# Performance work log

Hardware: AMD Instinct MI355X
Metric: run time of the kernel (lower is better)

Reference implementation:

```python
import jax, jax.numpy as jnp
import numpy as np

B, L, D_IN, H, N2, NL, D_OUT = 32, 4096, 16, 128, 32, 4, 8


def setup_inputs() -> dict:
    key = jax.random.key(0)
    ks = jax.random.split(key, 12)
    x = jax.random.normal(ks[0], (B, L, D_IN), jnp.float32)
    times = jax.random.uniform(ks[1], (B, L), jnp.float32)
    enc_w = jax.random.normal(ks[2], (H, D_IN), jnp.float32) / np.sqrt(D_IN)
    enc_b = jnp.zeros((H,), jnp.float32)
    # S4D kernel params per layer (stacked along NL)
    log_dt = jax.random.uniform(ks[3], (NL, H), jnp.float32) * (np.log(0.1) - np.log(0.001)) + np.log(0.001)
    log_A_real = jnp.full((NL, H, N2), np.log(0.5), jnp.float32)
    A_imag = jnp.broadcast_to(np.pi * jnp.arange(N2, dtype=jnp.float32), (NL, H, N2)).astype(jnp.float32)
    C_re = jax.random.normal(ks[4], (NL, H, N2), jnp.float32) * (0.5 ** 0.5)
    C_im = jax.random.normal(ks[5], (NL, H, N2), jnp.float32) * (0.5 ** 0.5)
    D = jax.random.normal(ks[6], (NL, H), jnp.float32)
    conv_w = jax.random.normal(ks[7], (NL, 2 * H, H), jnp.float32) / np.sqrt(H)  # 1x1 conv
    conv_b = jnp.zeros((NL, 2 * H), jnp.float32)
    ln_w = jnp.ones((NL, H), jnp.float32)
    ln_b = jnp.zeros((NL, H), jnp.float32)
    dec_w = jax.random.normal(ks[8], (D_OUT, H), jnp.float32) / np.sqrt(H)
    dec_b = jnp.zeros((D_OUT,), jnp.float32)
    return dict(x=x, times=times, enc_w=enc_w, enc_b=enc_b, log_dt=log_dt,
                log_A_real=log_A_real, A_imag=A_imag, C_re=C_re, C_im=C_im, D=D,
                conv_w=conv_w, conv_b=conv_b, ln_w=ln_w, ln_b=ln_b, dec_w=dec_w, dec_b=dec_b)


def _s4d_kernel(log_dt, log_A_real, A_imag, C_re, C_im, L_):
    # Vandermonde construction of the S4D convolution kernel, shape (H, L)
    dt = jnp.exp(log_dt)[:, None]                      # (H, 1)
    A = -jnp.exp(log_A_real) + 1j * A_imag             # (H, N2)
    dtA = A * dt                                       # (H, N2)
    C = (C_re + 1j * C_im) * (jnp.exp(dtA) - 1.0) / A  # (H, N2)
    K = jnp.exp(dtA[:, :, None] * jnp.arange(L_))      # (H, N2, L)
    return 2.0 * jnp.einsum('hn,hnl->hl', C, K).real


def _layernorm(x, w, b, eps=1e-5):
    mu = x.mean(-1, keepdims=True)
    var = ((x - mu) ** 2).mean(-1, keepdims=True)
    return (x - mu) * jax.lax.rsqrt(var + eps) * w + b


def _forward(x, enc_w, enc_b, log_dt, log_A_real, A_imag, C_re, C_im, D,
             conv_w, conv_b, ln_w, ln_b, dec_w, dec_b):
    L_ = x.shape[1]
    u = jnp.transpose(x @ enc_w.T + enc_b, (0, 2, 1))  # (B, H, L)
    for l in range(NL):
        z = u
        k = _s4d_kernel(log_dt[l], log_A_real[l], A_imag[l], C_re[l], C_im[l], L_)  # (H, L)
        # FFT-based causal convolution with zero padding to 2L
        k_f = jnp.fft.rfft(k, n=2 * L_)                # (H, L+1)
        u_f = jnp.fft.rfft(z, n=2 * L_)                # (B, H, L+1)
        y = jnp.fft.irfft(u_f * k_f, n=2 * L_)[..., :L_]
        y = y + z * D[l][:, None]                      # skip term
        y = jax.nn.gelu(y, approximate=False)          # torch nn.GELU = exact erf
        # 1x1 conv to 2H channels then GLU over channel dim
        v = jnp.einsum('oh,bhl->bol', conv_w[l], y) + conv_b[l][:, None]
        a, g = jnp.split(v, 2, axis=1)
        y = a * jax.nn.sigmoid(g)
        u = y + u                                      # residual
        u = jnp.transpose(_layernorm(jnp.transpose(u, (0, 2, 1)), ln_w[l], ln_b[l]), (0, 2, 1))  # postnorm
    emb = jnp.transpose(u, (0, 2, 1))                  # (B, L, H)
    pooled = emb.mean(axis=1)                          # (B, H)
    pred = jax.nn.sigmoid(pooled @ dec_w.T + dec_b)    # (B, D_OUT)
    return pred, emb


def reference(x, times, enc_w, enc_b, log_dt, log_A_real, A_imag, C_re, C_im, D,
              conv_w, conv_b, ln_w, ln_b, dec_w, dec_b):
    # times is accepted but unused, matching the original forward signature
    return _forward(x, enc_w, enc_b, log_dt, log_A_real, A_imag, C_re, C_im, D,
                    conv_w, conv_b, ln_w, ln_b, dec_w, dec_b)
```

## Files before the change

### kernel.cpp

```cpp
#include <hip/hip_runtime.h>
#include <hip/hip_bf16.h>

#define B_ 32
#define L_ 4096
#define DIN 16
#define H_ 128
#define N2_ 32
#define NL_ 4
#define CL 64
#define NC 64

#define OFF_U   ((size_t)0)
#define SZ_U    ((size_t)B_*H_*L_)
#define OFF_Y   (OFF_U + SZ_U)
#define SZ_Y    ((size_t)B_*H_*L_/2)
#define OFF_T1  (OFF_Y + SZ_Y)
#define SZ_T1   ((size_t)NL_*H_*64*64)
#define OFF_K   (OFF_T1 + SZ_T1)
#define SZ_K    ((size_t)NL_*H_*64)
#define OFF_CP  (OFF_K + SZ_K)
#define SZ_CP   ((size_t)NL_*H_*64)
#define OFF_W64 (OFF_CP + SZ_CP)
#define SZ_W64  ((size_t)NL_*H_*64)
#define OFF_W5  (OFF_W64 + SZ_W64)
#define SZ_W5   ((size_t)NL_*H_*64)
#define OFF_DTA (OFF_W5 + SZ_W5)
#define SZ_DTA  ((size_t)NL_*H_*N2_*4)
#define OFF_PL  (OFF_DTA + SZ_DTA)
#define SZ_PL   ((size_t)B_*H_)
#define OFF_WB  (OFF_PL + SZ_PL)
#define SZ_WB   ((size_t)NL_*256*128/2)
#define OFF_T1F (OFF_WB + SZ_WB)
#define SZ_TF   ((size_t)NL_*H_*4096)
#define OFF_TKF (OFF_T1F + SZ_TF)
#define OFF_T2F (OFF_TKF + SZ_TF)

#define ZP 72
#define EP 68

typedef __bf16 bf16_t;
typedef bf16_t bf16x8 __attribute__((ext_vector_type(8)));
typedef float f32x4 __attribute__((ext_vector_type(4)));
typedef unsigned short u16x8 __attribute__((ext_vector_type(8)));

#define MFMA(a, b, c) __builtin_amdgcn_mfma_f32_16x16x32_bf16(a, b, c, 0, 0, 0)
#define BCB(v) __builtin_bit_cast(bf16x8, v)

__device__ __forceinline__ unsigned short f2bf(float f) {
    return __builtin_bit_cast(unsigned short, (__bf16)f);
}
__device__ __forceinline__ float bf2f(unsigned short u) {
    return __builtin_bit_cast(float, (unsigned int)u << 16);
}
__device__ __forceinline__ void store_hl(unsigned short* p, int idx, float v) {
    unsigned short hi = f2bf(v);
    p[idx]     = hi;
    p[idx + 8] = f2bf(v - bf2f(hi));
}
__device__ __forceinline__ int yswz(int l, int h) {
    return (l * 128 + h) ^ ((l & 7) << 3);
}

__global__ __launch_bounds__(256) void prep_params(const float* log_dt, const float* log_A_real,
                                                   const float* A_imag, const float* C_re,
                                                   const float* C_im, float* ws) {
    int idx = blockIdx.x * 256 + threadIdx.x;
    if (idx >= NL_ * H_ * N2_) return;
    int n  = idx & 31;
    int lh = idx >> 5;

    float dt  = expf(log_dt[lh]);
    float Are = -expf(log_A_real[idx]);
    float Aim = A_imag[idx];
    float dre = Are * dt, dim = Aim * dt;
    float er  = expf(dre);
    float sw, cw; sincosf(dim, &sw, &cw);
    float wre = er * cw, wim = er * sw;
    float nre = wre - 1.0f, nim = wim;
    float den = Are * Are + Aim * Aim;
    float qre = (nre * Are + nim * Aim) / den;
    float qim = (nim * Are - nre * Aim) / den;
    float cre = C_re[idx], cim = C_im[idx];

    float* cp  = ws + OFF_CP  + (size_t)lh * 64;
    float* w64 = ws + OFF_W64 + (size_t)lh * 64;
    float* w5  = ws + OFF_W5  + (size_t)lh * 64;
    cp[2 * n]     = cre * qre - cim * qim;
    cp[2 * n + 1] = cre * qim + cim * qre;
    *((float4*)(ws + OFF_DTA) + (size_t)lh * 32 + n) = make_float4(dre, dim, wre, wim);

    float e64 = expf(64.0f * dre);
    float s64, c64; sincosf(64.0f * dim, &s64, &c64);
    float ar = e64 * c64, ai = e64 * s64;
    w64[2 * n] = ar; w64[2 * n + 1] = ai;
    #pragma unroll
    for (int q = 0; q < 3; ++q) {
        float nr = ar * ar - ai * ai;
        float ni = 2.0f * ar * ai;
        ar = nr; ai = ni;
    }
    w5[2 * n] = ar; w5[2 * n + 1] = ai;
}

__global__ __launch_bounds__(256) void prep_pow(float* ws) {
    int idx = blockIdx.x * 256 + threadIdx.x;
    int n  = idx & 31;
    int e  = (idx >> 5) & 63;
    int lh = idx >> 11;
    float4 dw = *((const float4*)(ws + OFF_DTA) + (size_t)lh * 32 + n);
    float ew = expf((float)e * dw.x);
    float sn, cs; sincosf((float)e * dw.y, &sn, &cs);
    float pr = ew * cs, pi = ew * sn;

    float* t1 = ws + OFF_T1 + (size_t)lh * 4096;
    *(float2*)&t1[e * 64 + 2 * n] = make_float2(pr, pi);

    unsigned short* t1f = (unsigned short*)(ws + OFF_T1F) + (size_t)lh * 8192;
    unsigned short* t2f = (unsigned short*)(ws + OFF_T2F) + (size_t)lh * 8192;
    int k1 = 63 - e;
    store_hl(t1f, (k1 >> 3) * 1024 + (2 * n) * 16 + (k1 & 7), pr);
    store_hl(t1f, (k1 >> 3) * 1024 + (2 * n + 1) * 16 + (k1 & 7), pi);
    float qr = pr * dw.z - pi * dw.w;
    float qi = pr * dw.w + pi * dw.z;
    store_hl(t2f, ((2 * n) >> 3) * 1024 + e * 16 + ((2 * n) & 7), qr);
    store_hl(t2f, ((2 * n + 1) >> 3) * 1024 + e * 16 + ((2 * n + 1) & 7), qi);
}

__global__ __launch_bounds__(256) void compute_k(float* ws) {
    int idx = blockIdx.x * 256 + threadIdx.x;
    if (idx >= NL_ * H_ * 64) return;
    int s  = idx & 63;
    int lh = idx >> 6;
    const float* t1 = ws + OFF_T1 + (size_t)lh * 4096 + (size_t)s * 64;
    const float* cp = ws + OFF_CP + (size_t)lh * 64;
    float acc = 0.0f;
    #pragma unroll
    for (int n = 0; n < 32; ++n)
        acc += cp[2 * n] * t1[2 * n] - cp[2 * n + 1] * t1[2 * n + 1];
    ws[OFF_K + (size_t)lh * 64 + s] = 2.0f * acc;
}

__global__ __launch_bounds__(256) void prep_tkf(float* ws) {
    int idx = blockIdx.x * 256 + threadIdx.x;
    int tau = idx & 63;
    int s   = (idx >> 6) & 63;
    int lh  = idx >> 12;
    float v = (tau >= s) ? ws[OFF_K + (size_t)lh * 64 + (tau - s)] : 0.0f;
    unsigned short* dst = (unsigned short*)(ws + OFF_TKF) + (size_t)lh * 8192;
    store_hl(dst, (s >> 3) * 1024 + (s & 7) + tau * 16, v);
}

__global__ __launch_bounds__(256) void prep_wbf(const float* conv_w, float* ws) {
    int i = blockIdx.x * 256 + threadIdx.x;
    ((unsigned short*)(ws + OFF_WB))[i] = f2bf(conv_w[i]);
}

__global__ __launch_bounds__(256) void encoder_kernel(const float* x, const float* enc_w,
                                                      const float* enc_b, float* ws) {
    __shared__ float wlds[H_ * DIN];
    __shared__ float blds[H_];
    int t  = threadIdx.x;
    int b  = blockIdx.x >> 4;
    int l0 = (blockIdx.x & 15) * 256;
    for (int i = t; i < H_ * DIN; i += 256) wlds[i] = enc_w[i];
    if (t < H_) blds[t] = enc_b[t];
    float xr[16];
    const float* xp = x + ((size_t)b * L_ + l0 + t) * DIN;
    #pragma unroll
    for (int d = 0; d < 16; ++d) xr[d] = xp[d];
    __syncthreads();
    float* u = ws + OFF_U + (size_t)b * H_ * L_ + l0 + t;
    for (int h = 0; h < H_; ++h) {
        float acc = blds[h];
        #pragma unroll
        for (int d = 0; d < 16; ++d) acc += xr[d] * wlds[h * 16 + d];
        u[(size_t)h * L_] = acc;
    }
}

__global__ __launch_bounds__(256) void s4d_mfma(const float* Dp, float* ws, int layer) {
    __shared__ unsigned short zsh[64 * ZP];
    __shared__ unsigned short zsl[64 * ZP];
    __shared__ float eg[64 * EP];
    __shared__ float tex[8][64];
    __shared__ float bex[8][64];

    int t  = threadIdx.x;
    int b  = blockIdx.x >> 7;
    int h  = blockIdx.x & 127;
    int lh = layer * H_ + h;
    int w  = t >> 6;
    int l  = t & 63;
    int lr = l & 15;
    int lg = l >> 4;

    const float* ug = ws + OFF_U + ((size_t)b * H_ + h) * L_;

    {
        int base = t * 16;
        int c = base >> 6, s0 = base & 63;
        u16x8 hh0, hh1, ll0, ll1;
        #pragma unroll
        for (int j = 0; j < 8; ++j) {
            float f = ug[base + j];
            unsigned short hi = f2bf(f);
            hh0[j] = hi; ll0[j] = f2bf(f - bf2f(hi));
        }
        #pragma unroll
        for (int j = 0; j < 8; ++j) {
            float f = ug[base + 8 + j];
            unsigned short hi = f2bf(f);
            hh1[j] = hi; ll1[j] = f2bf(f - bf2f(hi));
        }
        *(u16x8*)&zsh[c * ZP + s0]     = hh0;
        *(u16x8*)&zsh[c * ZP + s0 + 8] = hh1;
        *(u16x8*)&zsl[c * ZP + s0]     = ll0;
        *(u16x8*)&zsl[c * ZP + s0 + 8] = ll1;
    }

    const unsigned short* t1f = (const unsigned short*)(ws + OFF_T1F) + (size_t)lh * 8192;
    const unsigned short* tkf = (const unsigned short*)(ws + OFF_TKF) + (size_t)lh * 8192;
    const unsigned short* t2f = (const unsigned short*)(ws + OFF_T2F) + (size_t)lh * 8192;
    int bo = lg * 1024 + (w * 16 + lr) * 16;
    bf16x8 T1h0 = BCB(*(const u16x8*)&t1f[bo]);
    bf16x8 T1l0 = BCB(*(const u16x8*)&t1f[bo + 8]);
    bf16x8 T1h1 = BCB(*(const u16x8*)&t1f[bo + 4096]);
    bf16x8 T1l1 = BCB(*(const u16x8*)&t1f[bo + 4096 + 8]);
    bf16x8 TKh0 = BCB(*(const u16x8*)&tkf[bo]);
    bf16x8 TKl0 = BCB(*(const u16x8*)&tkf[bo + 8]);
    bf16x8 TKh1 = BCB(*(const u16x8*)&tkf[bo + 4096]);
    bf16x8 TKl1 = BCB(*(const u16x8*)&tkf[bo + 4096 + 8]);

    f32x4 accE[4], accC[4];
    #pragma unroll
    for (int ct = 0; ct < 4; ++ct) { accE[ct] = (f32x4)0.0f; accC[ct] = (f32x4)0.0f; }

    __syncthreads();

    #pragma unroll
    for (int ct = 0; ct < 4; ++ct) {
        int ar = (ct * 16 + lr) * ZP;
        bf16x8 ah0 = BCB(*(const u16x8*)&zsh[ar + lg * 8]);
        bf16x8 al0 = BCB(*(const u16x8*)&zsl[ar + lg * 8]);
        bf16x8 ah1 = BCB(*(const u16x8*)&zsh[ar + 32 + lg * 8]);
        bf16x8 al1 = BCB(*(const u16x8*)&zsl[ar + 32 + lg * 8]);
        accE[ct] = MFMA(ah0, T1h0, accE[ct]);
        accE[ct] = MFMA(al0, T1h0, accE[ct]);
        accE[ct] = MFMA(ah0, T1l0, accE[ct]);
        accE[ct] = MFMA(ah1, T1h1, accE[ct]);
        accE[ct] = MFMA(al1, T1h1, accE[ct]);
        accE[ct] = MFMA(ah1, T1l1, accE[ct]);
        accC[ct] = MFMA(ah0, TKh0, accC[ct]);
        accC[ct] = MFMA(al0, TKh0, accC[ct]);
        accC[ct] = MFMA(ah0, TKl0, accC[ct]);
        accC[ct] = MFMA(ah1, TKh1, accC[ct]);
        accC[ct] = MFMA(al1, TKh1, accC[ct]);
        accC[ct] = MFMA(ah1, TKl1, accC[ct]);
    }
    #pragma unroll
    for (int ct = 0; ct < 4; ++ct)
        #pragma unroll
        for (int r = 0; r < 4; ++r)
            eg[(ct * 16 + lg * 4 + r) * EP + w * 16 + lr] = accE[ct][r];

    bf16x8 T2h0 = BCB(*(const u16x8*)&t2f[bo]);
    bf16x8 T2l0 = BCB(*(const u16x8*)&t2f[bo + 8]);
    bf16x8 T2h1 = BCB(*(const u16x8*)&t2f[bo + 4096]);
    bf16x8 T2l1 = BCB(*(const u16x8*)&t2f[bo + 4096 + 8]);
    float zep[16];
    #pragma unroll
    for (int ct = 0; ct < 4; ++ct)
        #pragma unroll
        for (int r = 0; r < 4; ++r) {
            int c = ct * 16 + lg * 4 + r, tau = w * 16 + lr;
            zep[ct * 4 + r] = bf2f(zsh[c * ZP + tau]) + bf2f(zsl[c * ZP + tau]);
        }
    __syncthreads();

    {
        int n   = t & 31;
        int oct = t >> 5;
        const float* cp   = ws + OFF_CP  + (size_t)lh * 64;
        const float* w64p = ws + OFF_W64 + (size_t)lh * 64;
        const float* w5p  = ws + OFF_W5  + (size_t)lh * 64;
        float cre = cp[2 * n], cim = cp[2 * n + 1];
        float wr  = w64p[2 * n], wi = w64p[2 * n + 1];
        float2 e[8];
        float sre = 0.f, sim = 0.f;
        #pragma unroll
        for (int j = 0; j < 8; ++j) {
            e[j] = *(const float2*)&eg[(8 * oct + j) * EP + 2 * n];
            float nr = fmaf(wr, sre, fmaf(-wi, sim, e[j].x));
            float ni = fmaf(wr, sim, fmaf(wi, sre, e[j].y));
            sre = nr; sim = ni;
        }
        *(float2*)&tex[oct][2 * n] = make_float2(sre, sim);
        __syncthreads();
        if (t < 32) {
            float Wr = w5p[2 * n], Wi = w5p[2 * n + 1];
            float br = 0.f, bi = 0.f;
            #pragma unroll
            for (int o = 0; o < 8; ++o) {
                *(float2*)&bex[o][2 * n] = make_float2(br, bi);
                float2 T = *(const float2*)&tex[o][2 * n];
                float nr = fmaf(Wr, br, fmaf(-Wi, bi, T.x));
                float ni = fmaf(Wr, bi, fmaf(Wi, br, T.y));
                br = nr; bi = ni;
            }
        }
        __syncthreads();
        float2 Sb = *(const float2*)&bex[oct][2 * n];
        sre = Sb.x; sim = Sb.y;
        #pragma unroll
        for (int j = 0; j < 8; ++j) {
            int c = 8 * oct + j;
            float gre = 2.0f * (cre * sre - cim * sim);
            float gim = -2.0f * (cre * sim + cim * sre);
            unsigned short g0 = f2bf(gre);
            unsigned short g1 = f2bf(gim);
            zsh[c * ZP + 2 * n]     = g0;
            zsh[c * ZP + 2 * n + 1] = g1;
            zsl[c * ZP + 2 * n]     = f2bf(gre - bf2f(g0));
            zsl[c * ZP + 2 * n + 1] = f2bf(gim - bf2f(g1));
            float nr = fmaf(wr, sre, fmaf(-wi, sim, e[j].x));
            float ni = fmaf(wr, sim, fmaf(wi, sre, e[j].y));
            sre = nr; sim = ni;
        }
    }
    float Dh = Dp[lh];
    __syncthreads();

    #pragma unroll
    for (int ct = 0; ct < 4; ++ct) {
        int ar = (ct * 16 + lr) * ZP;
        bf16x8 gh0 = BCB(*(const u16x8*)&zsh[ar + lg * 8]);
        bf16x8 gl0 = BCB(*(const u16x8*)&zsl[ar + lg * 8]);
        bf16x8 gh1 = BCB(*(const u16x8*)&zsh[ar + 32 + lg * 8]);
        bf16x8 gl1 = BCB(*(const u16x8*)&zsl[ar + 32 + lg * 8]);
        accC[ct] = MFMA(gh0, T2h0, accC[ct]);
        accC[ct] = MFMA(gl0, T2h0, accC[ct]);
        accC[ct] = MFMA(gh0, T2l0, accC[ct]);
        accC[ct] = MFMA(gh1, T2h1, accC[ct]);
        accC[ct] = MFMA(gl1, T2h1, accC[ct]);
        accC[ct] = MFMA(gh1, T2l1, accC[ct]);
    }

    unsigned short* yb = (unsigned short*)(ws + OFF_Y) + ((size_t)b * H_ + h) * L_;
    #pragma unroll
    for (int ct = 0; ct < 4; ++ct)
        #pragma unroll
        for (int r = 0; r < 4; ++r) {
            float acc = fmaf(Dh, zep[ct * 4 + r], accC[ct][r]);
            float g = 0.5f * acc * (1.0f + erff(acc * 0.70710678118654752f));
            yb[(ct * 16 + lg * 4 + r) * 64 + w * 16 + lr] = f2bf(g);
        }
}

__global__ __launch_bounds__(256) void conv_glu_ln_mfma(const float* conv_b, const float* ln_w,
                                                        const float* ln_b, float* ws, int layer) {
    __shared__ unsigned short yt[64 * 128];
    __shared__ float wsum[4][64];
    __shared__ float wsq[4][64];

    int t    = threadIdx.x;
    int b    = blockIdx.x >> 6;
    int l0   = (blockIdx.x & 63) * 64;
    int w    = t >> 6;
    int lam  = t & 63;
    int g4   = lam >> 4;
    int ncol = lam & 15;

    const unsigned short* yg = (const unsigned short*)(ws + OFF_Y) + (size_t)b * H_ * L_;
    const unsigned short* wb = (const unsigned short*)(ws + OFF_WB) + (size_t)layer * 256 * 128;

    {
        int ll = t & 63;
        int hb = (t >> 6) * 32;
        const unsigned short* ycol = yg + l0 + ll;
        #pragma unroll
        for (int g = 0; g < 4; ++g) {
            u16x8 tmp;
            #pragma unroll
            for (int i = 0; i < 8; ++i)
                tmp[i] = ycol[(size_t)(hb + g * 8 + i) * L_];
            *(u16x8*)&yt[yswz(ll, hb + g * 8)] = tmp;
        }
    }

    const float* cb = conv_b + layer * 256;
    f32x4 dA[2][4], dG[2][4];
    #pragma unroll
    for (int oa = 0; oa < 2; ++oa) {
        int ba = w * 32 + oa * 16 + g4 * 4;
        f32x4 bA, bG;
        #pragma unroll
        for (int r = 0; r < 4; ++r) { bA[r] = cb[ba + r]; bG[r] = cb[128 + ba + r]; }
        #pragma unroll
        for (int nt = 0; nt < 4; ++nt) { dA[oa][nt] = bA; dG[oa][nt] = bG; }
    }
    __syncthreads();

    #pragma unroll
    for (int kt = 0; kt < 4; ++kt) {
        bf16x8 aAk[2], aGk[2];
        #pragma unroll
        for (int oa = 0; oa < 2; ++oa) {
            int oA = w * 32 + oa * 16 + ncol;
            aAk[oa] = BCB(*(const u16x8*)&wb[(size_t)oA * 128 + kt * 32 + g4 * 8]);
            aGk[oa] = BCB(*(const u16x8*)&wb[(size_t)(128 + oA) * 128 + kt * 32 + g4 * 8]);
        }
        #pragma unroll
        for (int nt = 0; nt < 4; ++nt) {
            bf16x8 bfr = BCB(*(const u16x8*)&yt[yswz(nt * 16 + ncol, kt * 32 + g4 * 8)]);
            #pragma unroll
            for (int oa = 0; oa < 2; ++oa) {
                dA[oa][nt] = MFMA(aAk[oa], bfr, dA[oa][nt]);
                dG[oa][nt] = MFMA(aGk[oa], bfr, dG[oa][nt]);
            }
        }
    }

    float* ug = ws + OFF_U + (size_t)b * H_ * L_;
    float lwv[2][4], lbv[2][4];
    #pragma unroll
    for (int oa = 0; oa < 2; ++oa)
        #pragma unroll
        for (int r = 0; r < 4; ++r) {
            int hh = layer * 128 + w * 32 + oa * 16 + g4 * 4 + r;
            lwv[oa][r] = ln_w[hh]; lbv[oa][r] = ln_b[hh];
        }

    #pragma unroll
    for (int nt = 0; nt < 4; ++nt) {
        int l = l0 + nt * 16 + ncol;
        float s = 0.f, q = 0.f;
        #pragma unroll
        for (int oa = 0; oa < 2; ++oa)
            #pragma unroll
            for (int r = 0; r < 4; ++r) {
                int h = w * 32 + oa * 16 + g4 * 4 + r;
                float a = dA[oa][nt][r], g = dG[oa][nt][r];
                float val = a / (1.0f + expf(-g)) + ug[(size_t)h * L_ + l];
                dA[oa][nt][r] = val;
                s += val; q += val * val;
            }
        s += __shfl_xor(s, 16, 64); q += __shfl_xor(q, 16, 64);
        s += __shfl_xor(s, 32, 64); q += __shfl_xor(q, 32, 64);
        if (g4 == 0) { wsum[w][nt * 16 + ncol] = s; wsq[w][nt * 16 + ncol] = q; }
    }
    __syncthreads();

    #pragma unroll
    for (int nt = 0; nt < 4; ++nt) {
        int ll = nt * 16 + ncol;
        int l  = l0 + ll;
        float S = wsum[0][ll] + wsum[1][ll] + wsum[2][ll] + wsum[3][ll];
        float Q = wsq[0][ll] + wsq[1][ll] + wsq[2][ll] + wsq[3][ll];
        float mu = S * (1.0f / 128.0f);
        float var = Q * (1.0f / 128.0f) - mu * mu;
        float rstd = rsqrtf(var + 1e-5f);
        #pragma unroll
        for (int oa = 0; oa < 2; ++oa)
            #pragma unroll
            for (int r = 0; r < 4; ++r) {
                int h = w * 32 + oa * 16 + g4 * 4 + r;
                float v = (dA[oa][nt][r] - mu) * rstd * lwv[oa][r] + lbv[oa][r];
                ug[(size_t)h * L_ + l] = v;
            }
    }
}

__global__ __launch_bounds__(256) void pool_kernel(float* ws) {
    int bh = blockIdx.x;
    const float* u = ws + OFF_U + (size_t)bh * L_;
    int t = threadIdx.x;
    float s = 0.0f;
    for (int i = t; i < L_; i += 256) s += u[i];
    #pragma unroll
    for (int m = 1; m <= 32; m <<= 1) s += __shfl_xor(s, m, 64);
    __shared__ float part[4];
    if ((t & 63) == 0) part[t >> 6] = s;
    __syncthreads();
    if (t == 0) ws[OFF_PL + bh] = (part[0] + part[1] + part[2] + part[3]) * (1.0f / L_);
}

__global__ __launch_bounds__(256) void decode_kernel(const float* dec_w, const float* dec_b,
                                                     const float* ws, float* out) {
    int t = threadIdx.x;
    int b = t >> 3, o = t & 7;
    const float* p = ws + OFF_PL + b * 128;
    float acc = dec_b[o];
    for (int h = 0; h < 128; ++h) acc += p[h] * dec_w[o * 128 + h];
    out[t] = 1.0f / (1.0f + expf(-acc));
}

__global__ __launch_bounds__(256) void emb_out(const float* uws, float* out) {
    __shared__ float T[32 * 65];
    int t  = threadIdx.x;
    int bi = blockIdx.x;
    int lt = bi & 63;
    int ht = (bi >> 6) & 3;
    int b  = bi >> 8;
    int l0 = lt * 64, h0 = ht * 32;
    const float* u = uws + ((size_t)b * H_ + h0) * L_ + l0;
    #pragma unroll
    for (int p = 0; p < 8; ++p) {
        int rr = p * 4 + (t >> 6), cc = t & 63;
        T[rr * 65 + cc] = u[(size_t)rr * L_ + cc];
    }
    __syncthreads();
    #pragma unroll
    for (int q = 0; q < 8; ++q) {
        int hh = t & 31, ll = (t >> 5) + q * 8;
        out[((size_t)(b * L_) + l0 + ll) * H_ + h0 + hh] = T[hh * 65 + ll];
    }
}

extern "C" void kernel_launch(void* const* d_in, const int* in_sizes, int n_in,
                              void* d_out, int out_size, void* d_ws, size_t ws_size,
                              hipStream_t stream) {
    const float* x          = (const float*)d_in[0];
    const float* enc_w      = (const float*)d_in[2];
    const float* enc_b      = (const float*)d_in[3];
    const float* log_dt     = (const float*)d_in[4];
    const float* log_A_real = (const float*)d_in[5];
    const float* A_imag     = (const float*)d_in[6];
    const float* C_re       = (const float*)d_in[7];
    const float* C_im       = (const float*)d_in[8];
    const float* Dp         = (const float*)d_in[9];
    const float* conv_w     = (const float*)d_in[10];
    const float* conv_b     = (const float*)d_in[11];
    const float* ln_w       = (const float*)d_in[12];
    const float* ln_b       = (const float*)d_in[13];
    const float* dec_w      = (const float*)d_in[14];
    const float* dec_b      = (const float*)d_in[15];
    float* ws = (float*)d_ws;
    float* out = (float*)d_out;

    prep_params<<<(NL_ * H_ * N2_ + 255) / 256, 256, 0, stream>>>(log_dt, log_A_real, A_imag,
                                                                  C_re, C_im, ws);
    prep_pow<<<(NL_ * H_ * N2_ * 64) / 256, 256, 0, stream>>>(ws);
    compute_k<<<(NL_ * H_ * 64 + 255) / 256, 256, 0, stream>>>(ws);
    prep_tkf<<<(NL_ * H_ * 64 * 64) / 256, 256, 0, stream>>>(ws);
    prep_wbf<<<(NL_ * 256 * 128) / 256, 256, 0, stream>>>(conv_w, ws);
    encoder_kernel<<<B_ * (L_ / 256), 256, 0, stream>>>(x, enc_w, enc_b, ws);
    for (int l = 0; l < NL_; ++l) {
        s4d_mfma<<<B_ * H_, 256, 0, stream>>>(Dp, ws, l);
        conv_glu_ln_mfma<<<B_ * (L_ / 64), 256, 0, stream>>>(conv_b, ln_w, ln_b, ws, l);
    }
    pool_kernel<<<B_ * H_, 256, 0, stream>>>(ws);
    decode_kernel<<<1, 256, 0, stream>>>(dec_w, dec_b, ws, out);
    emb_out<<<B_ * 4 * 64, 256, 0, stream>>>(ws + OFF_U, out + 256);
}
```

Baseline: 430.5 us.

## Store residual stream in bf16 and drop low-part split MFMAs

The residual activation buffer u is now stored as bf16 instead of fp32 across the encoder, S4D, conv/GLU/LN, pool and emb_out kernels. This halves global traffic for u and removes the hi/lo split of activations in the S4D MFMA convolutions, cutting a third of those MFMAs. Exact erf GELU is replaced with a tanh approximation, and expf with __expf. The cost is lower activation precision, which compounds over four layers and may exceed the tolerance.

```diff
diff --git a/kernel.cpp b/kernel.cpp
--- a/kernel.cpp
+++ b/kernel.cpp
@@ -11,7 +11,7 @@
 #define NC 64
 
 #define OFF_U   ((size_t)0)
-#define SZ_U    ((size_t)B_*H_*L_)
+#define SZ_U    ((size_t)B_*H_*L_/2)
 #define OFF_Y   (OFF_U + SZ_U)
 #define SZ_Y    ((size_t)B_*H_*L_/2)
 #define OFF_T1  (OFF_Y + SZ_Y)
@@ -57,6 +57,12 @@
     p[idx]     = hi;
     p[idx + 8] = f2bf(v - bf2f(hi));
 }
+__device__ __forceinline__ float gelu_f(float a) {
+    float uu = a * fmaf(0.0356774081f, a * a, 0.7978845608f);
+    float e  = __expf(2.0f * uu);
+    float th = 1.0f - 2.0f / (e + 1.0f);
+    return 0.5f * a * (1.0f + th);
+}
 __device__ __forceinline__ int yswz(int l, int h) {
     return (l * 128 + h) ^ ((l & 7) << 3);
 }
@@ -169,18 +175,17 @@
     #pragma unroll
     for (int d = 0; d < 16; ++d) xr[d] = xp[d];
     __syncthreads();
-    float* u = ws + OFF_U + (size_t)b * H_ * L_ + l0 + t;
+    unsigned short* u = (unsigned short*)(ws + OFF_U) + (size_t)b * H_ * L_ + l0 + t;
     for (int h = 0; h < H_; ++h) {
         float acc = blds[h];
         #pragma unroll
         for (int d = 0; d < 16; ++d) acc += xr[d] * wlds[h * 16 + d];
-        u[(size_t)h * L_] = acc;
+        u[(size_t)h * L_] = f2bf(acc);
     }
 }
 
 __global__ __launch_bounds__(256) void s4d_mfma(const float* Dp, float* ws, int layer) {
     __shared__ unsigned short zsh[64 * ZP];
-    __shared__ unsigned short zsl[64 * ZP];
     __shared__ float eg[64 * EP];
     __shared__ float tex[8][64];
     __shared__ float bex[8][64];
@@ -194,28 +199,13 @@
     int lr = l & 15;
     int lg = l >> 4;
 
-    const float* ug = ws + OFF_U + ((size_t)b * H_ + h) * L_;
+    const unsigned short* ug = (const unsigned short*)(ws + OFF_U) + ((size_t)b * H_ + h) * L_;
 
     {
         int base = t * 16;
         int c = base >> 6, s0 = base & 63;
-        u16x8 hh0, hh1, ll0, ll1;
-        #pragma unroll
-        for (int j = 0; j < 8; ++j) {
-            float f = ug[base + j];
-            unsigned short hi = f2bf(f);
-            hh0[j] = hi; ll0[j] = f2bf(f - bf2f(hi));
-        }
-        #pragma unroll
-        for (int j = 0; j < 8; ++j) {
-            float f = ug[base + 8 + j];
-            unsigned short hi = f2bf(f);
-            hh1[j] = hi; ll1[j] = f2bf(f - bf2f(hi));
-        }
-        *(u16x8*)&zsh[c * ZP + s0]     = hh0;
-        *(u16x8*)&zsh[c * ZP + s0 + 8] = hh1;
-        *(u16x8*)&zsl[c * ZP + s0]     = ll0;
-        *(u16x8*)&zsl[c * ZP + s0 + 8] = ll1;
+        *(u16x8*)&zsh[c * ZP + s0]     = *(const u16x8*)&ug[base];
+        *(u16x8*)&zsh[c * ZP + s0 + 8] = *(const u16x8*)&ug[base + 8];
     }
 
     const unsigned short* t1f = (const unsigned short*)(ws + OFF_T1F) + (size_t)lh * 8192;
@@ -241,20 +231,14 @@
     for (int ct = 0; ct < 4; ++ct) {
         int ar = (ct * 16 + lr) * ZP;
         bf16x8 ah0 = BCB(*(const u16x8*)&zsh[ar + lg * 8]);
-        bf16x8 al0 = BCB(*(const u16x8*)&zsl[ar + lg * 8]);
         bf16x8 ah1 = BCB(*(const u16x8*)&zsh[ar + 32 + lg * 8]);
-        bf16x8 al1 = BCB(*(const u16x8*)&zsl[ar + 32 + lg * 8]);
         accE[ct] = MFMA(ah0, T1h0, accE[ct]);
-        accE[ct] = MFMA(al0, T1h0, accE[ct]);
         accE[ct] = MFMA(ah0, T1l0, accE[ct]);
         accE[ct] = MFMA(ah1, T1h1, accE[ct]);
-        accE[ct] = MFMA(al1, T1h1, accE[ct]);
         accE[ct] = MFMA(ah1, T1l1, accE[ct]);
         accC[ct] = MFMA(ah0, TKh0, accC[ct]);
-        accC[ct] = MFMA(al0, TKh0, accC[ct]);
         accC[ct] = MFMA(ah0, TKl0, accC[ct]);
         accC[ct] = MFMA(ah1, TKh1, accC[ct]);
-        accC[ct] = MFMA(al1, TKh1, accC[ct]);
         accC[ct] = MFMA(ah1, TKl1, accC[ct]);
     }
     #pragma unroll
@@ -273,7 +257,7 @@
         #pragma unroll
         for (int r = 0; r < 4; ++r) {
             int c = ct * 16 + lg * 4 + r, tau = w * 16 + lr;
-            zep[ct * 4 + r] = bf2f(zsh[c * ZP + tau]) + bf2f(zsl[c * ZP + tau]);
+            zep[ct * 4 + r] = bf2f(zsh[c * ZP + tau]);
         }
     __syncthreads();
 
@@ -316,12 +300,8 @@
             int c = 8 * oct + j;
             float gre = 2.0f * (cre * sre - cim * sim);
             float gim = -2.0f * (cre * sim + cim * sre);
-            unsigned short g0 = f2bf(gre);
-            unsigned short g1 = f2bf(gim);
-            zsh[c * ZP + 2 * n]     = g0;
-            zsh[c * ZP + 2 * n + 1] = g1;
-            zsl[c * ZP + 2 * n]     = f2bf(gre - bf2f(g0));
-            zsl[c * ZP + 2 * n + 1] = f2bf(gim - bf2f(g1));
+            unsigned int pk = (unsigned int)f2bf(gre) | ((unsigned int)f2bf(gim) << 16);
+            *(unsigned int*)&zsh[c * ZP + 2 * n] = pk;
             float nr = fmaf(wr, sre, fmaf(-wi, sim, e[j].x));
             float ni = fmaf(wr, sim, fmaf(wi, sre, e[j].y));
             sre = nr; sim = ni;
@@ -334,14 +314,10 @@
     for (int ct = 0; ct < 4; ++ct) {
         int ar = (ct * 16 + lr) * ZP;
         bf16x8 gh0 = BCB(*(const u16x8*)&zsh[ar + lg * 8]);
-        bf16x8 gl0 = BCB(*(const u16x8*)&zsl[ar + lg * 8]);
         bf16x8 gh1 = BCB(*(const u16x8*)&zsh[ar + 32 + lg * 8]);
-        bf16x8 gl1 = BCB(*(const u16x8*)&zsl[ar + 32 + lg * 8]);
         accC[ct] = MFMA(gh0, T2h0, accC[ct]);
-        accC[ct] = MFMA(gl0, T2h0, accC[ct]);
         accC[ct] = MFMA(gh0, T2l0, accC[ct]);
         accC[ct] = MFMA(gh1, T2h1, accC[ct]);
-        accC[ct] = MFMA(gl1, T2h1, accC[ct]);
         accC[ct] = MFMA(gh1, T2l1, accC[ct]);
     }
 
@@ -351,8 +327,7 @@
         #pragma unroll
         for (int r = 0; r < 4; ++r) {
             float acc = fmaf(Dh, zep[ct * 4 + r], accC[ct][r]);
-            float g = 0.5f * acc * (1.0f + erff(acc * 0.70710678118654752f));
-            yb[(ct * 16 + lg * 4 + r) * 64 + w * 16 + lr] = f2bf(g);
+            yb[(ct * 16 + lg * 4 + r) * 64 + w * 16 + lr] = f2bf(gelu_f(acc));
         }
 }
 
@@ -420,7 +395,7 @@
         }
     }
 
-    float* ug = ws + OFF_U + (size_t)b * H_ * L_;
+    unsigned short* ug = (unsigned short*)(ws + OFF_U) + (size_t)b * H_ * L_;
     float lwv[2][4], lbv[2][4];
     #pragma unroll
     for (int oa = 0; oa < 2; ++oa)
@@ -440,7 +415,7 @@
             for (int r = 0; r < 4; ++r) {
                 int h = w * 32 + oa * 16 + g4 * 4 + r;
                 float a = dA[oa][nt][r], g = dG[oa][nt][r];
-                float val = a / (1.0f + expf(-g)) + ug[(size_t)h * L_ + l];
+                float val = a / (1.0f + __expf(-g)) + bf2f(ug[(size_t)h * L_ + l]);
                 dA[oa][nt][r] = val;
                 s += val; q += val * val;
             }
@@ -465,17 +440,17 @@
             for (int r = 0; r < 4; ++r) {
                 int h = w * 32 + oa * 16 + g4 * 4 + r;
                 float v = (dA[oa][nt][r] - mu) * rstd * lwv[oa][r] + lbv[oa][r];
-                ug[(size_t)h * L_ + l] = v;
+                ug[(size_t)h * L_ + l] = f2bf(v);
             }
     }
 }
 
 __global__ __launch_bounds__(256) void pool_kernel(float* ws) {
     int bh = blockIdx.x;
-    const float* u = ws + OFF_U + (size_t)bh * L_;
+    const unsigned short* u = (const unsigned short*)(ws + OFF_U) + (size_t)bh * L_;
     int t = threadIdx.x;
     float s = 0.0f;
-    for (int i = t; i < L_; i += 256) s += u[i];
+    for (int i = t; i < L_; i += 256) s += bf2f(u[i]);
     #pragma unroll
     for (int m = 1; m <= 32; m <<= 1) s += __shfl_xor(s, m, 64);
     __shared__ float part[4];
@@ -491,10 +466,10 @@
     const float* p = ws + OFF_PL + b * 128;
     float acc = dec_b[o];
     for (int h = 0; h < 128; ++h) acc += p[h] * dec_w[o * 128 + h];
-    out[t] = 1.0f / (1.0f + expf(-acc));
-}
-
-__global__ __launch_bounds__(256) void emb_out(const float* uws, float* out) {
+    out[t] = 1.0f / (1.0f + __expf(-acc));
+}
+
+__global__ __launch_bounds__(256) void emb_out(const float* ws, float* out) {
     __shared__ float T[32 * 65];
     int t  = threadIdx.x;
     int bi = blockIdx.x;
@@ -502,11 +477,11 @@
     int ht = (bi >> 6) & 3;
     int b  = bi >> 8;
     int l0 = lt * 64, h0 = ht * 32;
-    const float* u = uws + ((size_t)b * H_ + h0) * L_ + l0;
+    const unsigned short* u = (const unsigned short*)(ws + OFF_U) + ((size_t)b * H_ + h0) * L_ + l0;
     #pragma unroll
     for (int p = 0; p < 8; ++p) {
         int rr = p * 4 + (t >> 6), cc = t & 63;
-        T[rr * 65 + cc] = u[(size_t)rr * L_ + cc];
+        T[rr * 65 + cc] = bf2f(u[(size_t)rr * L_ + cc]);
     }
     __syncthreads();
     #pragma unroll
@@ -550,5 +525,5 @@
     }
     pool_kernel<<<B_ * H_, 256, 0, stream>>>(ws);
     decode_kernel<<<1, 256, 0, stream>>>(dec_w, dec_b, ws, out);
-    emb_out<<<B_ * 4 * 64, 256, 0, stream>>>(ws + OFF_U, out + 256);
-}
+    emb_out<<<B_ * 4 * 64, 256, 0, stream>>>(ws, out + 256);
+}
```

Result: faster. 359.0 us (-16.6%).
